# Kernel optimization log

Measured on AMD Instinct MI355X. Metric: run time of the kernel, lower is better.

Reference implementation:

```python
import jax, jax.numpy as jnp
import numpy as np

SIGMA_DATA = 16.0
ALPHA_BOND = 1.0


def safe_norm(x, axis=-1):
    # L2 norm with zero (sub)gradient at 0, matching torch.norm's behavior
    sq = jnp.sum(x * x, axis=axis)
    n = jnp.sqrt(jnp.where(sq > 0, sq, 1.0))
    return jnp.where(sq > 0, n, 0.0)


def weighted_rigid_align(x_l, xGT_l, w_l):
    # Aligns x_l onto xGT_l's frame (Kabsch with weights); output is detached.
    wm = w_l[..., None]                                   # [B,N,1]
    denom = jnp.sum(wm, axis=1, keepdims=True)
    mu = jnp.sum(wm * x_l, axis=1, keepdims=True) / denom
    muGT = jnp.sum(wm * xGT_l, axis=1, keepdims=True) / denom
    xc = x_l - mu
    xGTc = xGT_l - muGT
    # M = (w * xGT_c)^T @ x_c  -> [B,3,3]
    M = jnp.einsum('bni,bnj->bij', wm * xGTc, xc)
    U, S, Vh = jnp.linalg.svd(M)
    R = U @ Vh
    det = jnp.linalg.det(R)
    Fm = jnp.array([[1.0, 0.0, 0.0], [0.0, 1.0, 0.0], [0.0, 0.0, -1.0]], dtype=R.dtype)
    Rfix = jnp.einsum('bij,jk,bkl->bil', U, Fm, Vh)
    R = jnp.where(det[:, None, None] < 0, Rfix, R)
    xalign = xc @ jnp.swapaxes(R, -1, -2) + muGT
    return jax.lax.stop_gradient(xalign)


def diffusion_loss(xpred_l, xGT_l, ht, w_l):
    # Align ground truth onto prediction (note arg order in original forward)
    xGT_aligned = weighted_rigid_align(xGT_l, xpred_l, w_l)
    loss = jnp.sum(safe_norm(xpred_l - xGT_aligned) * w_l) / jnp.sum(w_l)
    if ALPHA_BOND > 0:
        w_pair = w_l[:, :, None] * w_l[:, None, :]                 # [B,N,N]
        d_pred = safe_norm(xpred_l[:, :, None] - xpred_l[:, None]) # [B,N,N]
        d_gt = safe_norm(xGT_l[:, :, None] - xGT_l[:, None])       # [B,N,N]
        L_bond = w_pair * (d_pred - d_gt) ** 2
        loss = loss + ALPHA_BOND * jnp.sum(L_bond) / jnp.sum(w_pair)
    return (ht ** 2 + SIGMA_DATA ** 2) / (ht + SIGMA_DATA) ** 2 * loss


def setup_inputs() -> dict:
    key = jax.random.key(0)
    k1, k2, k3, k4 = jax.random.split(key, 4)
    B, N = 4, 2048
    xpred_l = jax.random.normal(k1, (B, N, 3), dtype=jnp.float32) * 10.0
    xGT_l = jax.random.normal(k2, (B, N, 3), dtype=jnp.float32) * 10.0
    ht = jax.random.uniform(k3, (B,), dtype=jnp.float32, minval=0.1, maxval=4.0)
    w_l = jax.random.uniform(k4, (B, N), dtype=jnp.float32, minval=0.1, maxval=1.0)
    return {"xpred_l": xpred_l, "xGT_l": xGT_l, "ht": ht, "w_l": w_l}


def reference(xpred_l, xGT_l, ht, w_l):
    return diffusion_loss(xpred_l, xGT_l, ht, w_l)
```

## Files before the change

kernel.cpp:

```cpp
#include <hip/hip_runtime.h>
#include <math.h>


#define RT 256
#define CT 64
#define MAXB 8
#define MAXGX 16

__global__ __launch_bounds__(RT, 4)
void k_bond_stats(const float* __restrict__ pred, const float* __restrict__ gt,
                  const float* __restrict__ w, double* __restrict__ ws,
                  int N, int B) {
    const int b    = blockIdx.z;
    const int bx   = blockIdx.x;
    const int r0   = bx * RT;
    const int c0   = blockIdx.y * CT;
    const int tid  = threadIdx.x;
    const int lane = tid & 63, wave = tid >> 6;
    const int GX   = gridDim.x;
    const unsigned linear = (blockIdx.z * gridDim.y + blockIdx.y) * GX + blockIdx.x;

    double* statsSlot = ws;
    double* bondSlot  = ws + (size_t)B * GX * 16;

    const float* p  = pred + (size_t)b * N * 3;
    const float* g  = gt   + (size_t)b * N * 3;
    const float* wb = w    + (size_t)b * N;

    __shared__ float4 sp4[CT], sg4[CT];
    __shared__ double shred[4][16];

    const int  n      = r0 + tid;
    const bool row_ok = (n < N);
    float px=0.f,py=0.f,pz=0.f,gx=0.f,gy=0.f,gz=0.f,wn=0.f;
    if (row_ok) {
        px = p[3*n]; py = p[3*n+1]; pz = p[3*n+2];
        gx = g[3*n]; gy = g[3*n+1]; gz = g[3*n+2];
        wn = wb[n];
    }

    const bool bond_active = (c0 + CT > r0 + 1) && (c0 < N);
    float bond_f = 0.0f;
    if (bond_active) {
        for (int i = tid; i < CT; i += RT) {
            int m = c0 + i;
            float4 a = make_float4(0.f,0.f,0.f,0.f), c = a;
            if (m < N) {
                a = make_float4(p[3*m], p[3*m+1], p[3*m+2], wb[m]);
                c = make_float4(g[3*m], g[3*m+1], g[3*m+2], 0.f);
            }
            sp4[i] = a; sg4[i] = c;
        }
        __syncthreads();
        if (row_ok) {
            const int cc = min(CT, N - c0);
            if (c0 >= r0 + RT) {
                #pragma unroll 4
                for (int i = 0; i < cc; i++) {
                    float4 cp = sp4[i], cg = sg4[i];
                    float dxp=px-cp.x, dyp=py-cp.y, dzp=pz-cp.z;
                    float dxg=gx-cg.x, dyg=gy-cg.y, dzg=gz-cg.z;
                    float dp = sqrtf(dxp*dxp+dyp*dyp+dzp*dzp);
                    float dg = sqrtf(dxg*dxg+dyg*dyg+dzg*dzg);
                    float dd = dp - dg;
                    bond_f += (wn*cp.w)*(dd*dd);
                }
            } else if (n < c0 + cc - 1) {
                #pragma unroll 4
                for (int i = 0; i < cc; i++) {
                    float4 cp = sp4[i], cg = sg4[i];
                    float dxp=px-cp.x, dyp=py-cp.y, dzp=pz-cp.z;
                    float dxg=gx-cg.x, dyg=gy-cg.y, dzg=gz-cg.z;
                    float dp = sqrtf(dxp*dxp+dyp*dyp+dzp*dzp);
                    float dg = sqrtf(dxg*dxg+dyg*dyg+dzg*dzg);
                    float dd = dp - dg;
                    float t  = (wn*cp.w)*(dd*dd);
                    bond_f += (c0 + i > n) ? t : 0.0f;
                }
            }
        }
    }
    bond_f *= 2.0f;

    if (blockIdx.y == 0) {
        double wd=wn, pxd=px,pyd=py,pzd=pz, gxd=gx,gyd=gy,gzd=gz;
        double st[16] = {wd, wd*pxd, wd*pyd, wd*pzd, wd*gxd, wd*gyd, wd*gzd,
                         wd*pxd*gxd, wd*pxd*gyd, wd*pxd*gzd,
                         wd*pyd*gxd, wd*pyd*gyd, wd*pyd*gzd,
                         wd*pzd*gxd, wd*pzd*gyd, wd*pzd*gzd};
        #pragma unroll
        for (int off = 32; off > 0; off >>= 1) {
            #pragma unroll
            for (int k = 0; k < 16; k++) st[k] += __shfl_down(st[k], off, 64);
        }
        if (lane == 0) {
            #pragma unroll
            for (int k = 0; k < 16; k++) shred[wave][k] = st[k];
        }
        __syncthreads();
        if (tid < 16)
            statsSlot[((size_t)b*GX + bx)*16 + tid] =
                shred[0][tid]+shred[1][tid]+shred[2][tid]+shred[3][tid];
        __syncthreads();
    }

    double bd = (double)bond_f;
    #pragma unroll
    for (int off = 32; off > 0; off >>= 1) bd += __shfl_down(bd, off, 64);
    if (lane == 0) shred[wave][0] = bd;
    __syncthreads();
    if (tid == 0)
        bondSlot[linear] = shred[0][0]+shred[1][0]+shred[2][0]+shred[3][0];
}

__global__ __launch_bounds__(RT, 1)
void k_tail(const float* __restrict__ pred, const float* __restrict__ gt,
            const float* __restrict__ ht, const float* __restrict__ w,
            float* __restrict__ out, const double* __restrict__ ws,
            int N, int B, int GX, unsigned total) {
    const int tid  = threadIdx.x;
    const int lane = tid & 63, wave = tid >> 6;
    const double* statsSlot = ws;
    const double* bondSlot  = ws + (size_t)B * GX * 16;

    __shared__ double sstat[MAXB][16];
    __shared__ double shred[4][16];
    __shared__ float  Rf[MAXB][15];
    __shared__ double Wd[MAXB];
    __shared__ double s_bond, s_loss;

    if (tid < B * 16) {
        int bb = tid >> 4, k = tid & 15;
        double acc = 0.0;
        for (int j = 0; j < GX; j++) acc += statsSlot[((size_t)bb*GX + j)*16 + k];
        sstat[bb][k] = acc;
    }

    double bsum = 0.0;
    for (unsigned i = tid; i < total; i += RT) bsum += bondSlot[i];
    #pragma unroll
    for (int off = 32; off > 0; off >>= 1) bsum += __shfl_down(bsum, off, 64);
    if (lane == 0) shred[wave][0] = bsum;
    __syncthreads();
    if (tid == 0) s_bond = shred[0][0]+shred[1][0]+shred[2][0]+shred[3][0];

    if (tid < B) {
        const double* s = sstat[tid];
        double W = s[0];
        double mup[3] = { s[1]/W, s[2]/W, s[3]/W };
        double mug[3] = { s[4]/W, s[5]/W, s[6]/W };
        double M[3][3];
        for (int i = 0; i < 3; i++)
            for (int j = 0; j < 3; j++)
                M[i][j] = s[7 + i*3 + j] - W * mup[i] * mug[j];
        double A[3][3];
        for (int i = 0; i < 3; i++)
            for (int j = 0; j < 3; j++) {
                double t = 0.0;
                for (int k = 0; k < 3; k++) t += M[k][i] * M[k][j];
                A[i][j] = t;
            }
        double V[3][3] = {{1,0,0},{0,1,0},{0,0,1}};
        for (int sweep = 0; sweep < 6; sweep++) {
            for (int pq = 0; pq < 3; pq++) {
                int pp_ = (pq == 2) ? 1 : 0;
                int qq_ = (pq == 0) ? 1 : 2;
                double apq = A[pp_][qq_];
                if (fabs(apq) < 1e-300) continue;
                double app = A[pp_][pp_], aqq = A[qq_][qq_];
                double theta = (aqq - app) / (2.0 * apq);
                double t = copysign(1.0, theta) / (fabs(theta) + sqrt(theta*theta + 1.0));
                double cj = 1.0 / sqrt(t*t + 1.0), sn = t * cj;
                A[pp_][pp_] = app - t * apq;
                A[qq_][qq_] = aqq + t * apq;
                A[pp_][qq_] = A[qq_][pp_] = 0.0;
                int r = 3 - pp_ - qq_;
                double arp = A[r][pp_], arq = A[r][qq_];
                A[r][pp_] = A[pp_][r] = cj*arp - sn*arq;
                A[r][qq_] = A[qq_][r] = sn*arp + cj*arq;
                for (int rr = 0; rr < 3; rr++) {
                    double vp = V[rr][pp_], vq = V[rr][qq_];
                    V[rr][pp_] = cj*vp - sn*vq;
                    V[rr][qq_] = sn*vp + cj*vq;
                }
            }
        }
        double d[3] = { A[0][0], A[1][1], A[2][2] };
        int idx[3] = {0, 1, 2};
        for (int i = 0; i < 2; i++)
            for (int j = i + 1; j < 3; j++)
                if (d[idx[j]] > d[idx[i]]) { int tt = idx[i]; idx[i] = idx[j]; idx[j] = tt; }
        double u[3][3], v[3][3];
        for (int i = 0; i < 3; i++) {
            int c_ = idx[i];
            double sv = sqrt(fmax(d[c_], 0.0));
            double inv = (sv > 1e-12) ? 1.0 / sv : 0.0;
            for (int r = 0; r < 3; r++) v[i][r] = V[r][c_];
            for (int r = 0; r < 3; r++) {
                double t = 0.0;
                for (int k = 0; k < 3; k++) t += M[r][k] * v[i][k];
                u[i][r] = t * inv;
            }
        }
        double detM = M[0][0]*(M[1][1]*M[2][2] - M[1][2]*M[2][1])
                    - M[0][1]*(M[1][0]*M[2][2] - M[1][2]*M[2][0])
                    + M[0][2]*(M[1][0]*M[2][1] - M[1][1]*M[2][0]);
        double sg2 = (detM < 0.0) ? -1.0 : 1.0;
        for (int r = 0; r < 3; r++)
            for (int cc2 = 0; cc2 < 3; cc2++)
                Rf[tid][r*3+cc2] = (float)(u[0][r]*v[0][cc2] + u[1][r]*v[1][cc2]
                                           + sg2 * u[2][r]*v[2][cc2]);
        for (int i = 0; i < 3; i++) Rf[tid][9 + i]  = (float)mup[i];
        for (int i = 0; i < 3; i++) Rf[tid][12 + i] = (float)mug[i];
        Wd[tid] = W;
    }
    __syncthreads();

    double al = 0.0;
    for (int bb = 0; bb < B; bb++) {
        float R0=Rf[bb][0], R1=Rf[bb][1], R2=Rf[bb][2];
        float R3=Rf[bb][3], R4=Rf[bb][4], R5=Rf[bb][5];
        float R6=Rf[bb][6], R7=Rf[bb][7], R8=Rf[bb][8];
        float mp0=Rf[bb][9],  mp1=Rf[bb][10], mp2=Rf[bb][11];
        float mg0=Rf[bb][12], mg1=Rf[bb][13], mg2=Rf[bb][14];
        const float* pp  = pred + (size_t)bb * N * 3;
        const float* gg  = gt   + (size_t)bb * N * 3;
        const float* wwb = w    + (size_t)bb * N;
        for (int nn = tid; nn < N; nn += RT) {
            float x0 = gg[3*nn]-mg0, x1 = gg[3*nn+1]-mg1, x2 = gg[3*nn+2]-mg2;
            float ax = fmaf(R0,x0, fmaf(R1,x1, fmaf(R2,x2, mp0)));
            float ay = fmaf(R3,x0, fmaf(R4,x1, fmaf(R5,x2, mp1)));
            float az = fmaf(R6,x0, fmaf(R7,x1, fmaf(R8,x2, mp2)));
            float ex = pp[3*nn]-ax, ey = pp[3*nn+1]-ay, ez = pp[3*nn+2]-az;
            float sq = ex*ex + ey*ey + ez*ez;
            al += (double)(wwb[nn] * sqrtf(sq));
        }
    }
    #pragma unroll
    for (int off = 32; off > 0; off >>= 1) al += __shfl_down(al, off, 64);
    if (lane == 0) shred[wave][1] = al;
    __syncthreads();
    if (tid == 0) {
        double at = shred[0][1]+shred[1][1]+shred[2][1]+shred[3][1];
        double tw = 0.0, twp = 0.0;
        for (int i = 0; i < B; i++) { double W = Wd[i]; tw += W; twp += W*W; }
        s_loss = at / tw + s_bond / twp;
    }
    __syncthreads();
    if (tid < B) {
        double h = (double)ht[tid];
        out[tid] = (float)(((h*h + 256.0) / ((h + 16.0)*(h + 16.0))) * s_loss);
    }
}

extern "C" void kernel_launch(void* const* d_in, const int* in_sizes, int n_in,
                              void* d_out, int out_size, void* d_ws, size_t ws_size,
                              hipStream_t stream) {
    const float* pred = (const float*)d_in[0];
    const float* gt   = (const float*)d_in[1];
    const float* ht   = (const float*)d_in[2];
    const float* w    = (const float*)d_in[3];
    int B = in_sizes[2];
    int N = in_sizes[3] / B;
    double* ws = (double*)d_ws;
    float* out = (float*)d_out;

    int gx = (N + RT - 1) / RT;
    int gy = (N + CT - 1) / CT;
    unsigned total = (unsigned)(gx * gy * B);

    k_bond_stats<<<dim3(gx, gy, B), dim3(RT), 0, stream>>>(pred, gt, w, ws, N, B);
    k_tail<<<dim3(1), dim3(RT), 0, stream>>>(pred, gt, ht, w, out, ws, N, B, gx, total);
}
```

Baseline: 98.74 us.

## Parallelize tail kernel across blocks with atomic finalize and widen bond column tile

The single-block tail kernel becomes a multi-block kernel (up to 64 blocks). Each block redundantly recomputes the per-batch SVD alignment, handles a slice of points and bond partials, and accumulates into global doubles with atomics. A last-block counter then does the final loss. Zeroing of the accumulators moves into the first kernel, and the bond column tile doubles to cut block count and partial slots. The catch is redundant SVD work per block, plus dependence on the first kernel's zeroing being ordered before the tail's atomics.

```diff
diff --git a/kernel.cpp b/kernel.cpp
--- a/kernel.cpp
+++ b/kernel.cpp
@@ -3,14 +3,13 @@
 
 
 #define RT 256
-#define CT 64
+#define CT 128
 #define MAXB 8
-#define MAXGX 16
 
 __global__ __launch_bounds__(RT, 4)
 void k_bond_stats(const float* __restrict__ pred, const float* __restrict__ gt,
                   const float* __restrict__ w, double* __restrict__ ws,
-                  int N, int B) {
+                  int N, int B, unsigned total) {
     const int b    = blockIdx.z;
     const int bx   = blockIdx.x;
     const int r0   = bx * RT;
@@ -22,6 +21,11 @@
 
     double* statsSlot = ws;
     double* bondSlot  = ws + (size_t)B * GX * 16;
+
+    if (blockIdx.x == 0 && blockIdx.y == 0 && blockIdx.z == 0 && tid == 0) {
+        double* fin = bondSlot + total;
+        fin[0] = 0.0; fin[1] = 0.0; fin[2] = 0.0;
+    }
 
     const float* p  = pred + (size_t)b * N * 3;
     const float* g  = gt   + (size_t)b * N * 3;
@@ -114,20 +118,26 @@
 }
 
 __global__ __launch_bounds__(RT, 1)
-void k_tail(const float* __restrict__ pred, const float* __restrict__ gt,
-            const float* __restrict__ ht, const float* __restrict__ w,
-            float* __restrict__ out, const double* __restrict__ ws,
-            int N, int B, int GX, unsigned total) {
+void k_tail2(const float* __restrict__ pred, const float* __restrict__ gt,
+             const float* __restrict__ ht, const float* __restrict__ w,
+             float* __restrict__ out, double* __restrict__ ws,
+             int N, int B, int GX, unsigned total, int AG) {
     const int tid  = threadIdx.x;
     const int lane = tid & 63, wave = tid >> 6;
     const double* statsSlot = ws;
     const double* bondSlot  = ws + (size_t)B * GX * 16;
+    double* fin = (double*)(bondSlot + total);
 
     __shared__ double sstat[MAXB][16];
-    __shared__ double shred[4][16];
-    __shared__ float  Rf[MAXB][15];
-    __shared__ double Wd[MAXB];
-    __shared__ double s_bond, s_loss;
+    __shared__ float  sR[MAXB][15];
+    __shared__ double sW[MAXB];
+    __shared__ double shredA[4], shredB[4];
+
+    float htv[MAXB];
+    if (tid == 0) {
+        #pragma unroll
+        for (int b2 = 0; b2 < MAXB; b2++) htv[b2] = (b2 < B) ? ht[b2] : 0.f;
+    }
 
     if (tid < B * 16) {
         int bb = tid >> 4, k = tid & 15;
@@ -137,12 +147,25 @@
     }
 
     double bsum = 0.0;
-    for (unsigned i = tid; i < total; i += RT) bsum += bondSlot[i];
-    #pragma unroll
-    for (int off = 32; off > 0; off >>= 1) bsum += __shfl_down(bsum, off, 64);
-    if (lane == 0) shred[wave][0] = bsum;
+    for (unsigned i = (unsigned)blockIdx.x * RT + tid; i < total; i += (unsigned)AG * RT)
+        bsum += bondSlot[i];
+
+    const int ptTotal = B * N;
+    const int stride  = AG * RT;
+    const int pt0     = blockIdx.x * RT + tid;
+    const bool have0  = (pt0 < ptTotal);
+    float px=0.f,py=0.f,pz=0.f,qx=0.f,qy=0.f,qz=0.f,wn=0.f;
+    int b0 = 0;
+    if (have0) {
+        b0 = pt0 / N; int n0 = pt0 - b0 * N;
+        const float* pp = pred + (size_t)b0 * N * 3;
+        const float* gg = gt   + (size_t)b0 * N * 3;
+        px = pp[3*n0]; py = pp[3*n0+1]; pz = pp[3*n0+2];
+        qx = gg[3*n0]; qy = gg[3*n0+1]; qz = gg[3*n0+2];
+        wn = w[(size_t)b0 * N + n0];
+    }
+
     __syncthreads();
-    if (tid == 0) s_bond = shred[0][0]+shred[1][0]+shred[2][0]+shred[3][0];
 
     if (tid < B) {
         const double* s = sstat[tid];
@@ -208,48 +231,66 @@
         double sg2 = (detM < 0.0) ? -1.0 : 1.0;
         for (int r = 0; r < 3; r++)
             for (int cc2 = 0; cc2 < 3; cc2++)
-                Rf[tid][r*3+cc2] = (float)(u[0][r]*v[0][cc2] + u[1][r]*v[1][cc2]
+                sR[tid][r*3+cc2] = (float)(u[0][r]*v[0][cc2] + u[1][r]*v[1][cc2]
                                            + sg2 * u[2][r]*v[2][cc2]);
-        for (int i = 0; i < 3; i++) Rf[tid][9 + i]  = (float)mup[i];
-        for (int i = 0; i < 3; i++) Rf[tid][12 + i] = (float)mug[i];
-        Wd[tid] = W;
+        for (int i = 0; i < 3; i++) sR[tid][9 + i]  = (float)mup[i];
+        for (int i = 0; i < 3; i++) sR[tid][12 + i] = (float)mug[i];
+        sW[tid] = W;
     }
     __syncthreads();
 
     double al = 0.0;
-    for (int bb = 0; bb < B; bb++) {
-        float R0=Rf[bb][0], R1=Rf[bb][1], R2=Rf[bb][2];
-        float R3=Rf[bb][3], R4=Rf[bb][4], R5=Rf[bb][5];
-        float R6=Rf[bb][6], R7=Rf[bb][7], R8=Rf[bb][8];
-        float mp0=Rf[bb][9],  mp1=Rf[bb][10], mp2=Rf[bb][11];
-        float mg0=Rf[bb][12], mg1=Rf[bb][13], mg2=Rf[bb][14];
-        const float* pp  = pred + (size_t)bb * N * 3;
-        const float* gg  = gt   + (size_t)bb * N * 3;
-        const float* wwb = w    + (size_t)bb * N;
-        for (int nn = tid; nn < N; nn += RT) {
-            float x0 = gg[3*nn]-mg0, x1 = gg[3*nn+1]-mg1, x2 = gg[3*nn+2]-mg2;
-            float ax = fmaf(R0,x0, fmaf(R1,x1, fmaf(R2,x2, mp0)));
-            float ay = fmaf(R3,x0, fmaf(R4,x1, fmaf(R5,x2, mp1)));
-            float az = fmaf(R6,x0, fmaf(R7,x1, fmaf(R8,x2, mp2)));
-            float ex = pp[3*nn]-ax, ey = pp[3*nn+1]-ay, ez = pp[3*nn+2]-az;
-            float sq = ex*ex + ey*ey + ez*ez;
-            al += (double)(wwb[nn] * sqrtf(sq));
-        }
-    }
+    if (have0) {
+        const float* Rb = sR[b0];
+        float x0 = qx - Rb[12], x1 = qy - Rb[13], x2 = qz - Rb[14];
+        float ax = fmaf(Rb[0],x0, fmaf(Rb[1],x1, fmaf(Rb[2],x2, Rb[9])));
+        float ay = fmaf(Rb[3],x0, fmaf(Rb[4],x1, fmaf(Rb[5],x2, Rb[10])));
+        float az = fmaf(Rb[6],x0, fmaf(Rb[7],x1, fmaf(Rb[8],x2, Rb[11])));
+        float ex = px-ax, ey = py-ay, ez = pz-az;
+        al += (double)(wn * sqrtf(ex*ex + ey*ey + ez*ez));
+    }
+    for (int pt = pt0 + stride; pt < ptTotal; pt += stride) {
+        int b2 = pt / N; int nn = pt - b2 * N;
+        const float* pp = pred + (size_t)b2 * N * 3;
+        const float* gg = gt   + (size_t)b2 * N * 3;
+        const float* Rb = sR[b2];
+        float x0 = gg[3*nn]-Rb[12], x1 = gg[3*nn+1]-Rb[13], x2 = gg[3*nn+2]-Rb[14];
+        float ax = fmaf(Rb[0],x0, fmaf(Rb[1],x1, fmaf(Rb[2],x2, Rb[9])));
+        float ay = fmaf(Rb[3],x0, fmaf(Rb[4],x1, fmaf(Rb[5],x2, Rb[10])));
+        float az = fmaf(Rb[6],x0, fmaf(Rb[7],x1, fmaf(Rb[8],x2, Rb[11])));
+        float ex = pp[3*nn]-ax, ey = pp[3*nn+1]-ay, ez = pp[3*nn+2]-az;
+        al += (double)(w[(size_t)b2*N + nn] * sqrtf(ex*ex + ey*ey + ez*ez));
+    }
+
     #pragma unroll
-    for (int off = 32; off > 0; off >>= 1) al += __shfl_down(al, off, 64);
-    if (lane == 0) shred[wave][1] = al;
+    for (int off = 32; off > 0; off >>= 1) {
+        al   += __shfl_down(al,   off, 64);
+        bsum += __shfl_down(bsum, off, 64);
+    }
+    if (lane == 0) { shredA[wave] = al; shredB[wave] = bsum; }
     __syncthreads();
+
     if (tid == 0) {
-        double at = shred[0][1]+shred[1][1]+shred[2][1]+shred[3][1];
-        double tw = 0.0, twp = 0.0;
-        for (int i = 0; i < B; i++) { double W = Wd[i]; tw += W; twp += W*W; }
-        s_loss = at / tw + s_bond / twp;
-    }
-    __syncthreads();
-    if (tid < B) {
-        double h = (double)ht[tid];
-        out[tid] = (float)(((h*h + 256.0) / ((h + 16.0)*(h + 16.0))) * s_loss);
+        double alB = shredA[0]+shredA[1]+shredA[2]+shredA[3];
+        double bB  = shredB[0]+shredB[1]+shredB[2]+shredB[3];
+        atomicAdd(&fin[0], alB);
+        atomicAdd(&fin[1], bB);
+        __threadfence();
+        unsigned old = atomicAdd((unsigned int*)&fin[2], 1u);
+        if (old == (unsigned)(AG - 1)) {
+            double at = atomicAdd(&fin[0], 0.0);
+            double bt = atomicAdd(&fin[1], 0.0);
+            double tw = 0.0, twp = 0.0;
+            for (int b2 = 0; b2 < B; b2++) { double W = sW[b2]; tw += W; twp += W*W; }
+            double loss = at / tw + bt / twp;
+            #pragma unroll
+            for (int b2 = 0; b2 < MAXB; b2++) {
+                if (b2 < B) {
+                    double h = (double)htv[b2];
+                    out[b2] = (float)(((h*h + 256.0) / ((h + 16.0)*(h + 16.0))) * loss);
+                }
+            }
+        }
     }
 }
 
@@ -269,6 +310,10 @@
     int gy = (N + CT - 1) / CT;
     unsigned total = (unsigned)(gx * gy * B);
 
-    k_bond_stats<<<dim3(gx, gy, B), dim3(RT), 0, stream>>>(pred, gt, w, ws, N, B);
-    k_tail<<<dim3(1), dim3(RT), 0, stream>>>(pred, gt, ht, w, out, ws, N, B, gx, total);
+    int ag = (B * N + RT - 1) / RT;
+    if (ag > 64) ag = 64;
+    if (ag < 1)  ag = 1;
+
+    k_bond_stats<<<dim3(gx, gy, B), dim3(RT), 0, stream>>>(pred, gt, w, ws, N, B, total);
+    k_tail2<<<dim3(ag), dim3(RT), 0, stream>>>(pred, gt, ht, w, out, ws, N, B, gx, total, ag);
 }
```

Result: no change. 97.52 us (-1.2%).
